# Kernel tuning notes

Hardware: AMD Instinct MI355X
Metric: run time of the kernel (lower is better)

## Reference

```python
import jax, jax.numpy as jnp
import numpy as np

N_NODES = 100000
N_EDGES = 3200000
IN_CH = 512
HID_CH = 40   # 2 * out_channels
OUT_CH = 20


def setup_inputs() -> dict:
    key = jax.random.key(0)
    k1, k2, k3, k4, k5, k6 = jax.random.split(key, 6)
    x = jax.random.normal(k1, (N_NODES, IN_CH), dtype=jnp.float32)
    edge_index = jax.random.randint(k2, (2, N_EDGES), 0, N_NODES, dtype=jnp.int32)
    # Glorot-style init for GCN weights, zero bias (PyG default)
    W1 = jax.random.normal(k3, (IN_CH, HID_CH), dtype=jnp.float32) * (1.0 / np.sqrt(IN_CH))
    b1 = jnp.zeros((HID_CH,), dtype=jnp.float32)
    W2 = jax.random.normal(k4, (HID_CH, OUT_CH), dtype=jnp.float32) * (1.0 / np.sqrt(HID_CH))
    b2 = jnp.zeros((OUT_CH,), dtype=jnp.float32)
    return {"x": x, "edge_index": edge_index, "W1": W1, "b1": b1, "W2": W2, "b2": b2}


def _gcn_conv(x, src, dst, W, b):
    """PyG GCNConv: add self-loops, symmetric norm, linear, scatter-add, bias."""
    n = x.shape[0]
    loops = jnp.arange(n, dtype=src.dtype)
    src = jnp.concatenate([src, loops])
    dst = jnp.concatenate([dst, loops])
    # in-degree over A + I (self-loops guarantee deg >= 1)
    deg = jax.ops.segment_sum(jnp.ones(src.shape[0], x.dtype), dst, num_segments=n)
    dinv = jax.lax.rsqrt(deg)
    norm = dinv[src] * dinv[dst]               # [E+N]
    h = x @ W                                   # [N, out] GEMM before aggregation
    msg = h[src] * norm[:, None]                # gather + scale
    out = jax.ops.segment_sum(msg, dst, num_segments=n)  # scatter-add at targets
    return out + b


def reference(x, edge_index, W1, b1, W2, b2):
    src, dst = edge_index[0], edge_index[1]
    h = jax.nn.relu(_gcn_conv(x, src, dst, W1, b1))
    # dropout is identity in eval mode (training=False)
    return _gcn_conv(h, src, dst, W2, b2)
```

## Files before the change

kernel.cpp:

```cpp
#include <hip/hip_runtime.h>
#include <cstddef>

static constexpr int NN   = 100000;
static constexpr int NE   = 3200000;
static constexpr int CIN  = 512;
static constexpr int CHID = 40;
static constexpr int COUT = 20;


__global__ __launch_bounds__(256) void k_count(const int* __restrict__ dst, int* __restrict__ cnt,
                                               int* __restrict__ rank, int n_edges4) {
  const int e4 = blockIdx.x * 256 + threadIdx.x;
  if (e4 >= n_edges4) return;
  const int4 d = ((const int4*)dst)[e4];
  int4 r;
  r.x = atomicAdd(&cnt[d.x], 1);
  r.y = atomicAdd(&cnt[d.y], 1);
  r.z = atomicAdd(&cnt[d.z], 1);
  r.w = atomicAdd(&cnt[d.w], 1);
  ((int4*)rank)[e4] = r;
}

__global__ __launch_bounds__(256) void k_scanA(const int* __restrict__ cnt, int* __restrict__ excl,
                                               int* __restrict__ bsums, float* __restrict__ dinv, int n) {
  __shared__ int sdata[256];
  const int t = threadIdx.x;
  const int base = blockIdx.x * 1024 + t * 4;
  int v[4];
#pragma unroll
  for (int j = 0; j < 4; ++j) {
    const int i = base + j;
    v[j] = (i < n) ? cnt[i] : 0;
    if (i < n) dinv[i] = rsqrtf((float)(v[j] + 1));
  }
  const int s4 = v[0] + v[1] + v[2] + v[3];
  sdata[t] = s4;
  __syncthreads();
  for (int off = 1; off < 256; off <<= 1) {
    int val = 0;
    if (t >= off) val = sdata[t - off];
    __syncthreads();
    sdata[t] += val;
    __syncthreads();
  }
  int run = sdata[t] - s4;
#pragma unroll
  for (int j = 0; j < 4; ++j) {
    const int i = base + j;
    if (i < n) excl[i] = run;
    run += v[j];
  }
  if (t == 255) bsums[blockIdx.x] = sdata[255];
}

__global__ __launch_bounds__(256) void k_scanB(int* __restrict__ bsums, int nb) {
  __shared__ int sdata[256];
  const int t = threadIdx.x;
  const int v = (t < nb) ? bsums[t] : 0;
  sdata[t] = v;
  __syncthreads();
  for (int off = 1; off < 256; off <<= 1) {
    int val = 0;
    if (t >= off) val = sdata[t - off];
    __syncthreads();
    sdata[t] += val;
    __syncthreads();
  }
  if (t < nb) bsums[t] = sdata[t] - v;
}

__global__ __launch_bounds__(256) void k_scanC(int* __restrict__ rowptr, const int* __restrict__ boff,
                                               int n, int n_edges) {
  const int i = blockIdx.x * 256 + threadIdx.x;
  if (i < n) rowptr[i] += boff[i >> 10];
  if (i == 0) rowptr[n] = n_edges;
}

__global__ __launch_bounds__(256) void k_fill(const int* __restrict__ src, const int* __restrict__ dst,
                                              const int* __restrict__ rank, const int* __restrict__ rowptr,
                                              int* __restrict__ csr_src, int n_edges4) {
  const int e4 = blockIdx.x * 256 + threadIdx.x;
  if (e4 >= n_edges4) return;
  const int4 s = ((const int4*)src)[e4];
  const int4 d = ((const int4*)dst)[e4];
  const int4 r = ((const int4*)rank)[e4];
  csr_src[rowptr[d.x] + r.x] = s.x;
  csr_src[rowptr[d.y] + r.y] = s.y;
  csr_src[rowptr[d.z] + r.z] = s.z;
  csr_src[rowptr[d.w] + r.w] = s.w;
}


__device__ __forceinline__ void consume16(float acc[CHID], const float4 cur[4],
                                          const float* __restrict__ Wb) {
#pragma unroll
  for (int j = 0; j < 4; ++j) {
    const float4 xv = cur[j];
    const float* __restrict__ Wk = Wb + j * 4 * CHID;
#pragma unroll
    for (int c = 0; c < CHID; ++c) {
      float a = acc[c];
      a = fmaf(xv.x, Wk[c], a);
      a = fmaf(xv.y, Wk[CHID + c], a);
      a = fmaf(xv.z, Wk[2 * CHID + c], a);
      a = fmaf(xv.w, Wk[3 * CHID + c], a);
      acc[c] = a;
    }
  }
}

__global__ __launch_bounds__(64) void k_gemm1(const float* __restrict__ x, const float* __restrict__ W,
                                              float* __restrict__ h, int n) {
  const int node = blockIdx.x * 64 + threadIdx.x;
  if (node >= n) return;
  const float4* __restrict__ x4 = (const float4*)(x + (size_t)node * CIN);
  float acc[CHID];
#pragma unroll
  for (int c = 0; c < CHID; ++c) acc[c] = 0.f;

  float4 cur[4], nxt[4];
#pragma unroll
  for (int j = 0; j < 4; ++j) cur[j] = x4[j];
  for (int b = 0; b < 31; ++b) {
#pragma unroll
    for (int j = 0; j < 4; ++j) nxt[j] = x4[(b + 1) * 4 + j];
    consume16(acc, cur, W + b * 16 * CHID);
#pragma unroll
    for (int j = 0; j < 4; ++j) cur[j] = nxt[j];
  }
  consume16(acc, cur, W + 31 * 16 * CHID);

  float* __restrict__ o = h + (size_t)node * CHID;
#pragma unroll
  for (int c = 0; c < CHID; ++c) o[c] = acc[c];
}

__global__ __launch_bounds__(256) void k_gemm2(const float* __restrict__ t1, const float* __restrict__ W,
                                               float* __restrict__ g, int n) {
  const int node = blockIdx.x * 256 + threadIdx.x;
  if (node >= n) return;
  const float4* __restrict__ r4 = (const float4*)(t1 + (size_t)node * CHID);
  float acc[COUT];
#pragma unroll
  for (int c = 0; c < COUT; ++c) acc[c] = 0.f;
#pragma unroll
  for (int kk = 0; kk < CHID / 4; ++kk) {
    const float4 xv = r4[kk];
    const float* __restrict__ Wk = W + kk * 4 * COUT;
#pragma unroll
    for (int c = 0; c < COUT; ++c) {
      float a = acc[c];
      a = fmaf(xv.x, Wk[c], a);
      a = fmaf(xv.y, Wk[COUT + c], a);
      a = fmaf(xv.z, Wk[2 * COUT + c], a);
      a = fmaf(xv.w, Wk[3 * COUT + c], a);
      acc[c] = a;
    }
  }
  float* __restrict__ o = g + (size_t)node * COUT;
#pragma unroll
  for (int c = 0; c < COUT; ++c) o[c] = acc[c];
}

__global__ __launch_bounds__(256) void k_agg40(const float* __restrict__ h, const int* __restrict__ rowptr,
                                               const int* __restrict__ csr_src, const float* __restrict__ dinv,
                                               const float* __restrict__ bias, float* __restrict__ out, int n) {
  const int wave = (blockIdx.x * 256 + (int)threadIdx.x) >> 6;
  const int lane = threadIdx.x & 63;
  const int sub  = lane / 20;
  const int cp   = lane % 20;
  const int node = wave * 3 + sub;
  if (sub >= 3 || node >= n) return;
  const float2* __restrict__ h2 = (const float2*)h;
  const int r0 = rowptr[node];
  const int r1 = rowptr[node + 1];
  const float dv = dinv[node];
  const float self_w = dv * dv;
  float2 acc = h2[(size_t)node * 20 + cp];
  acc.x *= self_w;
  acc.y *= self_w;
  int i = r0;
  for (; i + 4 <= r1; i += 4) {
    const int s0 = csr_src[i + 0];
    const int s1 = csr_src[i + 1];
    const int s2 = csr_src[i + 2];
    const int s3 = csr_src[i + 3];
    const float w0 = dinv[s0] * dv;
    const float w1 = dinv[s1] * dv;
    const float w2 = dinv[s2] * dv;
    const float w3 = dinv[s3] * dv;
    const float2 g0 = h2[(size_t)s0 * 20 + cp];
    const float2 g1 = h2[(size_t)s1 * 20 + cp];
    const float2 g2 = h2[(size_t)s2 * 20 + cp];
    const float2 g3 = h2[(size_t)s3 * 20 + cp];
    acc.x = fmaf(g0.x, w0, acc.x); acc.y = fmaf(g0.y, w0, acc.y);
    acc.x = fmaf(g1.x, w1, acc.x); acc.y = fmaf(g1.y, w1, acc.y);
    acc.x = fmaf(g2.x, w2, acc.x); acc.y = fmaf(g2.y, w2, acc.y);
    acc.x = fmaf(g3.x, w3, acc.x); acc.y = fmaf(g3.y, w3, acc.y);
  }
  for (; i < r1; ++i) {
    const int s = csr_src[i];
    const float w = dinv[s] * dv;
    const float2 g = h2[(size_t)s * 20 + cp];
    acc.x = fmaf(g.x, w, acc.x);
    acc.y = fmaf(g.y, w, acc.y);
  }
  const float2 bv = ((const float2*)bias)[cp];
  float2 v;
  v.x = fmaxf(acc.x + bv.x, 0.f);
  v.y = fmaxf(acc.y + bv.y, 0.f);
  ((float2*)out)[(size_t)node * 20 + cp] = v;
}

__global__ __launch_bounds__(256) void k_agg20(const float* __restrict__ h, const int* __restrict__ rowptr,
                                               const int* __restrict__ csr_src, const float* __restrict__ dinv,
                                               const float* __restrict__ bias, float* __restrict__ out, int n) {
  const int wave = (blockIdx.x * 256 + (int)threadIdx.x) >> 6;
  const int lane = threadIdx.x & 63;
  const int sub  = lane / 10;
  const int cp   = lane % 10;
  const int node = wave * 6 + sub;
  if (sub >= 6 || node >= n) return;
  const float2* __restrict__ h2 = (const float2*)h;
  const int r0 = rowptr[node];
  const int r1 = rowptr[node + 1];
  const float dv = dinv[node];
  const float self_w = dv * dv;
  float2 acc = h2[(size_t)node * 10 + cp];
  acc.x *= self_w;
  acc.y *= self_w;
  int i = r0;
  for (; i + 4 <= r1; i += 4) {
    const int s0 = csr_src[i + 0];
    const int s1 = csr_src[i + 1];
    const int s2 = csr_src[i + 2];
    const int s3 = csr_src[i + 3];
    const float w0 = dinv[s0] * dv;
    const float w1 = dinv[s1] * dv;
    const float w2 = dinv[s2] * dv;
    const float w3 = dinv[s3] * dv;
    const float2 g0 = h2[(size_t)s0 * 10 + cp];
    const float2 g1 = h2[(size_t)s1 * 10 + cp];
    const float2 g2 = h2[(size_t)s2 * 10 + cp];
    const float2 g3 = h2[(size_t)s3 * 10 + cp];
    acc.x = fmaf(g0.x, w0, acc.x); acc.y = fmaf(g0.y, w0, acc.y);
    acc.x = fmaf(g1.x, w1, acc.x); acc.y = fmaf(g1.y, w1, acc.y);
    acc.x = fmaf(g2.x, w2, acc.x); acc.y = fmaf(g2.y, w2, acc.y);
    acc.x = fmaf(g3.x, w3, acc.x); acc.y = fmaf(g3.y, w3, acc.y);
  }
  for (; i < r1; ++i) {
    const int s = csr_src[i];
    const float w = dinv[s] * dv;
    const float2 g = h2[(size_t)s * 10 + cp];
    acc.x = fmaf(g.x, w, acc.x);
    acc.y = fmaf(g.y, w, acc.y);
  }
  const float2 bv = ((const float2*)bias)[cp];
  float2 v;
  v.x = acc.x + bv.x;
  v.y = acc.y + bv.y;
  ((float2*)out)[(size_t)node * 10 + cp] = v;
}


extern "C" void kernel_launch(void* const* d_in, const int* in_sizes, int n_in,
                              void* d_out, int out_size, void* d_ws, size_t ws_size,
                              hipStream_t stream) {
  const float* x   = (const float*)d_in[0];
  const int*   ei  = (const int*)d_in[1];
  const float* W1  = (const float*)d_in[2];
  const float* b1  = (const float*)d_in[3];
  const float* W2  = (const float*)d_in[4];
  const float* b2  = (const float*)d_in[5];
  float* out = (float*)d_out;

  const int* srcp = ei;
  const int* dstp = ei + NE;

  char* ws = (char*)d_ws;
  size_t off = 0;
  auto take = [&](size_t bytes) -> char* {
    char* p = ws + off;
    off = (off + bytes + 255) & ~(size_t)255;
    return p;
  };
  int*   cnt     = (int*)take((size_t)NN * 4);
  int*   rowptr  = (int*)take((size_t)(NN + 1) * 4);
  float* dinv    = (float*)take((size_t)NN * 4);
  int*   bsums   = (int*)take(256 * 4);
  int*   rank    = (int*)take((size_t)NE * 4);
  int*   csr_src = (int*)take((size_t)NE * 4);
  float* h1      = (float*)take((size_t)NN * CHID * 4);
  float* t1      = (float*)take((size_t)NN * CHID * 4);
  float* g2      = h1;

  (void)in_sizes; (void)n_in; (void)out_size; (void)ws_size;

  hipMemsetAsync(cnt, 0, (size_t)NN * 4, stream);

  const int ne4 = NE / 4;
  k_count<<<(ne4 + 255) / 256, 256, 0, stream>>>(dstp, cnt, rank, ne4);
  const int nb = (NN + 1023) / 1024;
  k_scanA<<<nb, 256, 0, stream>>>(cnt, rowptr, bsums, dinv, NN);
  k_scanB<<<1, 256, 0, stream>>>(bsums, nb);
  k_scanC<<<(NN + 255) / 256, 256, 0, stream>>>(rowptr, bsums, NN, NE);
  k_fill<<<(ne4 + 255) / 256, 256, 0, stream>>>(srcp, dstp, rank, rowptr, csr_src, ne4);

  k_gemm1<<<(NN + 63) / 64, 64, 0, stream>>>(x, W1, h1, NN);
  const int nwaves1 = (NN + 2) / 3;
  k_agg40<<<(nwaves1 + 3) / 4, 256, 0, stream>>>(h1, rowptr, csr_src, dinv, b1, t1, NN);
  k_gemm2<<<(NN + 255) / 256, 256, 0, stream>>>(t1, W2, g2, NN);
  const int nwaves2 = (NN + 5) / 6;
  k_agg20<<<(nwaves2 + 3) / 4, 256, 0, stream>>>(g2, rowptr, csr_src, dinv, b2, out, NN);
}
```

Baseline: 786.8 us.

## Stage x tiles in swizzled LDS and split GEMM1 output columns across waves

Rewrites the first dense GEMM. It moves from one thread per node reading its own strided row to a 256-thread block that loads 64 rows of x coalesced into XOR-swizzled shared memory, 128 columns at a time. Each of the four waves then computes 10 of the 40 output channels for the 64 nodes. This is meant to fix the uncoalesced per-thread row reads and the 40-float accumulator pressure, trading them for extra syncthreads, LDS traffic and four times the W reads per node.

```diff
diff --git a/kernel.cpp b/kernel.cpp
--- a/kernel.cpp
+++ b/kernel.cpp
@@ -90,49 +90,62 @@
   csr_src[rowptr[d.w] + r.w] = s.w;
 }
 
-
-__device__ __forceinline__ void consume16(float acc[CHID], const float4 cur[4],
-                                          const float* __restrict__ Wb) {
-#pragma unroll
-  for (int j = 0; j < 4; ++j) {
-    const float4 xv = cur[j];
-    const float* __restrict__ Wk = Wb + j * 4 * CHID;
-#pragma unroll
-    for (int c = 0; c < CHID; ++c) {
-      float a = acc[c];
-      a = fmaf(xv.x, Wk[c], a);
-      a = fmaf(xv.y, Wk[CHID + c], a);
-      a = fmaf(xv.z, Wk[2 * CHID + c], a);
-      a = fmaf(xv.w, Wk[3 * CHID + c], a);
-      acc[c] = a;
+__global__ __launch_bounds__(256) void k_gemm1(const float* __restrict__ x, const float* __restrict__ W,
+                                               float* __restrict__ h, int n) {
+  __shared__ float xt[64 * 128];
+  const int t  = threadIdx.x;
+  const int nd = t & 63;
+  const int g  = __builtin_amdgcn_readfirstlane(t >> 6);
+  const int block0 = blockIdx.x * 64;
+
+  const int sn = t >> 5;
+  const int c4 = t & 31;
+
+  float acc[10];
+#pragma unroll
+  for (int j = 0; j < 10; ++j) acc[j] = 0.f;
+
+  for (int kt = 0; kt < 4; ++kt) {
+    float4 v[8];
+#pragma unroll
+    for (int r = 0; r < 8; ++r) {
+      const int row = r * 8 + sn;
+      int gn = block0 + row;
+      if (gn >= n) gn = n - 1;
+      v[r] = ((const float4*)(x + (size_t)gn * CIN + kt * 128))[c4];
     }
-  }
-}
-
-__global__ __launch_bounds__(64) void k_gemm1(const float* __restrict__ x, const float* __restrict__ W,
-                                              float* __restrict__ h, int n) {
-  const int node = blockIdx.x * 64 + threadIdx.x;
-  if (node >= n) return;
-  const float4* __restrict__ x4 = (const float4*)(x + (size_t)node * CIN);
-  float acc[CHID];
-#pragma unroll
-  for (int c = 0; c < CHID; ++c) acc[c] = 0.f;
-
-  float4 cur[4], nxt[4];
-#pragma unroll
-  for (int j = 0; j < 4; ++j) cur[j] = x4[j];
-  for (int b = 0; b < 31; ++b) {
-#pragma unroll
-    for (int j = 0; j < 4; ++j) nxt[j] = x4[(b + 1) * 4 + j];
-    consume16(acc, cur, W + b * 16 * CHID);
-#pragma unroll
-    for (int j = 0; j < 4; ++j) cur[j] = nxt[j];
-  }
-  consume16(acc, cur, W + 31 * 16 * CHID);
-
-  float* __restrict__ o = h + (size_t)node * CHID;
-#pragma unroll
-  for (int c = 0; c < CHID; ++c) o[c] = acc[c];
+    if (kt) __syncthreads();
+#pragma unroll
+    for (int r = 0; r < 8; ++r) {
+      const int row = r * 8 + sn;
+      const int byte = row * 512 + ((c4 * 16) ^ ((row & 31) << 4));
+      *(float4*)((char*)xt + byte) = v[r];
+    }
+    __syncthreads();
+
+    const float* __restrict__ Wg = W + (size_t)kt * 128 * CHID + g * 10;
+#pragma unroll 4
+    for (int k4 = 0; k4 < 32; ++k4) {
+      const int byte = nd * 512 + ((k4 * 16) ^ ((nd & 31) << 4));
+      const float4 xv = *(const float4*)((const char*)xt + byte);
+      const float* __restrict__ Wk = Wg + k4 * 4 * CHID;
+#pragma unroll
+      for (int j = 0; j < 10; ++j) acc[j] = fmaf(xv.x, Wk[j], acc[j]);
+#pragma unroll
+      for (int j = 0; j < 10; ++j) acc[j] = fmaf(xv.y, Wk[CHID + j], acc[j]);
+#pragma unroll
+      for (int j = 0; j < 10; ++j) acc[j] = fmaf(xv.z, Wk[2 * CHID + j], acc[j]);
+#pragma unroll
+      for (int j = 0; j < 10; ++j) acc[j] = fmaf(xv.w, Wk[3 * CHID + j], acc[j]);
+    }
+  }
+
+  const int node = block0 + nd;
+  if (node < n) {
+    float* __restrict__ o = h + (size_t)node * CHID + g * 10;
+#pragma unroll
+    for (int j = 0; j < 10; ++j) o[j] = acc[j];
+  }
 }
 
 __global__ __launch_bounds__(256) void k_gemm2(const float* __restrict__ t1, const float* __restrict__ W,
@@ -306,7 +319,7 @@
   k_scanC<<<(NN + 255) / 256, 256, 0, stream>>>(rowptr, bsums, NN, NE);
   k_fill<<<(ne4 + 255) / 256, 256, 0, stream>>>(srcp, dstp, rank, rowptr, csr_src, ne4);
 
-  k_gemm1<<<(NN + 63) / 64, 64, 0, stream>>>(x, W1, h1, NN);
+  k_gemm1<<<(NN + 63) / 64, 256, 0, stream>>>(x, W1, h1, NN);
   const int nwaves1 = (NN + 2) / 3;
   k_agg40<<<(nwaves1 + 3) / 4, 256, 0, stream>>>(h1, rowptr, csr_src, dinv, b1, t1, NN);
   k_gemm2<<<(NN + 255) / 256, 256, 0, stream>>>(t1, W2, g2, NN);
```

Result: slower. 835.8 us (+6.2%).
